# Kernel tuning notes

Hardware: AMD Instinct MI355X
Metric: run time of the kernel (lower is better)

The kernel has to match this reference:

```python
import jax, jax.numpy as jnp
import numpy as np

LN2 = 0.6931471805599453

def ssp(x):
    # 'shifted_sp' activation: softplus(x) - log(2)
    return jax.nn.softplus(x) - LN2

def _res_chain(x, W1, b1, W2, b2):
    # PhysNetResidual chain: x <- lin2(ssp(lin1(ssp(x)))) + x
    # W1/W2: [n_res, F, F], b1/b2: [n_res, F]
    for j in range(W1.shape[0]):
        h = ssp(x) @ W1[j] + b1[j]
        x = ssp(h) @ W2[j] + b2[j] + x
    return x

def _physnet_module(feat, radial_aev, idx12, p):
    (W_I, b_I, W_J, b_J, W_gate, gvec, W_int, b_int,
     ri_W1, ri_b1, ri_W2, ri_b2,
     ra_W1, ra_b1, ra_W2, ra_b2,
     ro_W1, ro_b1, ro_W2, ro_b2, W_out, b_out) = p
    N, F = feat.shape
    # self term (no species are dummy -> non_dummy indexing is identity)
    h_self = ssp(ssp(feat) @ W_I + b_I)                       # [N,F]
    # pair messages
    gate = radial_aev @ W_gate                                 # [P,F] (no bias)
    f12 = feat[idx12]                                          # [2,P,F] gather
    fm = ssp(ssp(f12) @ W_J + b_J)                             # [2,P,F]
    pair_msg = gate[None] * fm                                 # [2,P,F]
    proto = jnp.zeros_like(feat).at[idx12.reshape(-1)].add(
        pair_msg.reshape(-1, F))                               # scatter-add
    proto = proto + h_self
    msg = _res_chain(proto, ri_W1, ri_b1, ri_W2, ri_b2)
    feat2 = feat * gvec + ssp(msg) @ W_int + b_int
    feat2 = _res_chain(feat2, ra_W1, ra_b1, ra_W2, ra_b2)
    e = ssp(_res_chain(feat2, ro_W1, ro_b1, ro_W2, ro_b2)) @ W_out + b_out  # [N]
    return e, feat2

def setup_inputs() -> dict:
    key = jax.random.key(0)
    L, F, R = 5, 128, 64
    M, A = 128, 64
    N = M * A
    P = 400000
    ks = jax.random.split(key, 20)
    s = 0.05  # small weight scale keeps activations stable across 5 modules
    inp = {
        'species': jax.random.randint(ks[0], (M, A), 0, 4, dtype=jnp.int32),
        'features': jax.random.normal(ks[1], (N, F), jnp.float32),
        'radial_aev': jax.random.uniform(ks[2], (P, R), jnp.float32),
        'atom_index12': jax.random.randint(ks[3], (2, P), 0, N, dtype=jnp.int32),
        'W_I': jax.random.normal(ks[4], (L, F, F)) * s,
        'b_I': jnp.zeros((L, F)),
        'W_J': jax.random.normal(ks[5], (L, F, F)) * s,
        'b_J': jnp.zeros((L, F)),
        'W_gate': jax.random.normal(ks[6], (L, R, F)) * s,
        'gvec': jnp.ones((L, F)),
        'W_int': jax.random.normal(ks[7], (L, F, F)) * s,
        'b_int': jnp.zeros((L, F)),
        'ri_W1': jax.random.normal(ks[8], (L, 3, F, F)) * s,
        'ri_b1': jnp.zeros((L, 3, F)),
        'ri_W2': jax.random.normal(ks[9], (L, 3, F, F)) * s,
        'ri_b2': jnp.zeros((L, 3, F)),
        'ra_W1': jax.random.normal(ks[10], (L, 2, F, F)) * s,
        'ra_b1': jnp.zeros((L, 2, F)),
        'ra_W2': jax.random.normal(ks[11], (L, 2, F, F)) * s,
        'ra_b2': jnp.zeros((L, 2, F)),
        'ro_W1': jax.random.normal(ks[12], (L, 1, F, F)) * s,
        'ro_b1': jnp.zeros((L, 1, F)),
        'ro_W2': jax.random.normal(ks[13], (L, 1, F, F)) * s,
        'ro_b2': jnp.zeros((L, 1, F)),
        'W_out': jax.random.normal(ks[14], (L, F)) * s,
        'b_out': jnp.zeros((L,)),
    }
    return inp

def reference(species, features, radial_aev, atom_index12,
              W_I, b_I, W_J, b_J, W_gate, gvec, W_int, b_int,
              ri_W1, ri_b1, ri_W2, ri_b2,
              ra_W1, ra_b1, ra_W2, ra_b2,
              ro_W1, ro_b1, ro_W2, ro_b2, W_out, b_out):
    M, A = species.shape
    params = (W_I, b_I, W_J, b_J, W_gate, gvec, W_int, b_int,
              ri_W1, ri_b1, ri_W2, ri_b2,
              ra_W1, ra_b1, ra_W2, ra_b2,
              ro_W1, ro_b1, ro_W2, ro_b2, W_out, b_out)
    feat = features
    energies = jnp.zeros((M * A,), features.dtype)
    for l in range(W_I.shape[0]):  # fixed small module loop
        p = tuple(arr[l] for arr in params)
        e, feat = _physnet_module(feat, radial_aev, atom_index12, p)
        energies = energies + e
    return energies.reshape(M, A), feat
```

## Files before the change

kernel.cpp:

```cpp
#include <hip/hip_runtime.h>


#define LN2F 0.69314718055994530942f
#define NB 128

using short8  = __attribute__((ext_vector_type(8))) short;
using float4v = __attribute__((ext_vector_type(4))) float;
typedef const __attribute__((address_space(1))) unsigned int* gas1_t;
typedef __attribute__((address_space(3))) unsigned int* las3_t;

__device__ __forceinline__ float sspf(float x) {
  float ax = fabsf(x);
  return fmaxf(x, 0.0f) + __logf(1.0f + __expf(-ax)) - LN2F;
}

__device__ __forceinline__ unsigned short f2bf(float x) {
  return (unsigned short)((__float_as_uint(x) + 0x8000u) >> 16);
}

__device__ __forceinline__ unsigned short f2bf_ne(float x) {
  unsigned int u = __float_as_uint(x);
  u += 0x7fffu + ((u >> 16) & 1u);
  return (unsigned short)(u >> 16);
}

__device__ __forceinline__ void dma16(const void* g, void* l) {
  __builtin_amdgcn_global_load_lds((gas1_t)(unsigned long long)g,
                                   (las3_t)(unsigned long long)l, 16, 0, 0);
}

__device__ __forceinline__ void dma32k(const unsigned short* g, unsigned short* l,
                                       int w, int lane) {
  const char* gb = (const char*)g + w * 2048 + lane * 16;
  char* lb = (char*)l + w * 2048;
  dma16(gb, lb);
  dma16(gb + 1024, lb + 1024);
}
__device__ __forceinline__ void dma16k(const unsigned short* g, unsigned short* l,
                                       int w, int lane) {
  dma16((const char*)g + w * 1024 + lane * 16, (char*)l + w * 1024);
}

__global__ __launch_bounds__(256) void hist_pass(const int* __restrict__ idx,
                                                 unsigned int* __restrict__ H,
                                                 int n2p, int C) {
  __shared__ unsigned int h[8192];
  int b = blockIdx.x, tid = threadIdx.x;
  for (int i = tid; i < 8192; i += 256) h[i] = 0;
  __syncthreads();
  int s = b * C, e = min(s + C, n2p);
  for (int i = s + tid; i < e; i += 256) atomicAdd(&h[idx[i]], 1u);
  __syncthreads();
  for (int i = tid; i < 8192; i += 256) H[(size_t)b * 8192 + i] = h[i];
}

__global__ __launch_bounds__(256) void col_scan(unsigned int* __restrict__ H,
                                                unsigned int* __restrict__ tot) {
  int a = blockIdx.x * 256 + threadIdx.x;
  unsigned int run = 0;
  for (int b = 0; b < NB; ++b) {
    unsigned int v = H[(size_t)b * 8192 + a];
    H[(size_t)b * 8192 + a] = run;
    run += v;
  }
  tot[a] = run;
}

__global__ __launch_bounds__(256) void scan_kernel(const unsigned int* __restrict__ cnt,
                                                   unsigned int* __restrict__ off, int NA) {
  int t = threadIdx.x;
  unsigned int local[32], s = 0;
#pragma unroll
  for (int i = 0; i < 32; ++i) { local[i] = cnt[t * 32 + i]; s += local[i]; }
  unsigned int v = s;
  int lane = t & 63, w = t >> 6;
#pragma unroll
  for (int o = 1; o < 64; o <<= 1) {
    unsigned int u = __shfl_up(v, o, 64);
    if (lane >= o) v += u;
  }
  __shared__ unsigned int wt4[4];
  if (lane == 63) wt4[w] = v;
  __syncthreads();
  unsigned int base = 0;
  for (int k = 0; k < w; ++k) base += wt4[k];
  unsigned int excl = base + v - s;
#pragma unroll
  for (int i = 0; i < 32; ++i) { off[t * 32 + i] = excl; excl += local[i]; }
  if (t == 255) off[NA] = excl;
}

__global__ __launch_bounds__(256) void place_pass(const int* __restrict__ idx,
                                                  const unsigned int* __restrict__ H,
                                                  const unsigned int* __restrict__ off,
                                                  unsigned int* __restrict__ pairid,
                                                  int P, int C) {
  __shared__ unsigned int pos[8192];
  int b = blockIdx.x, tid = threadIdx.x;
  for (int i = tid; i < 8192; i += 256)
    pos[i] = off[i] + H[(size_t)b * 8192 + i];
  __syncthreads();
  int n2p = 2 * P;
  int s = b * C, e = min(s + C, n2p);
  for (int i = s + tid; i < e; i += 256) {
    int a = idx[i];
    unsigned int p = atomicAdd(&pos[a], 1u);
    pairid[p] = (i >= P) ? (unsigned int)(i - P) : (unsigned int)i;
  }
}

__global__ __launch_bounds__(256) void gather_kernel(const float* __restrict__ radial,
                                                     const unsigned int* __restrict__ off,
                                                     const unsigned int* __restrict__ pairid,
                                                     float* __restrict__ S) {
  __shared__ float red[3][64];
  int a = blockIdx.x;
  int lane = threadIdx.x & 63, w = threadIdx.x >> 6;
  unsigned int b = off[a], e = off[a + 1];
  float acc = 0.0f;
  for (unsigned int base = b + w; base < e; base += 32) {
    unsigned int pp[8];
    float vv[8];
#pragma unroll
    for (int k = 0; k < 8; ++k) {
      unsigned int j = base + 4 * k;
      pp[k] = pairid[j < e ? j : b];
    }
#pragma unroll
    for (int k = 0; k < 8; ++k) vv[k] = radial[(size_t)pp[k] * 64 + lane];
#pragma unroll
    for (int k = 0; k < 8; ++k) {
      unsigned int j = base + 4 * k;
      acc += (j < e) ? vv[k] : 0.0f;
    }
  }
  if (w > 0) red[w - 1][lane] = acc;
  __syncthreads();
  if (w == 0) {
    acc += red[0][lane] + red[1][lane] + red[2][lane];
    S[(size_t)a * 64 + lane] = acc;
  }
}

struct PrepArgs {
  const float* src[80];
  int isgate[80];
};

__global__ __launch_bounds__(256) void prep_weights(PrepArgs A, unsigned short* __restrict__ Wt) {
  int m = blockIdx.x;
  const float* s = A.src[m];
  unsigned short* d = Wt + (size_t)m * 16384;
  if (!A.isgate[m]) {
    for (int it = 0; it < 8; ++it) {
      int q = threadIdx.x + it * 256;
      int n = q & 127, j = q >> 7;
      unsigned short tmp[8];
#pragma unroll
      for (int cc = 0; cc < 8; ++cc) tmp[cc] = f2bf_ne(s[(8 * j + cc) * 128 + n]);
      *(uint4*)(d + (n * 16 + (j ^ (n & 15))) * 8) = *(uint4*)tmp;
    }
  } else {
    for (int it = 0; it < 4; ++it) {
      int q = threadIdx.x + it * 256;
      int n = q & 127, j = q >> 7;
      unsigned short tmp[8];
#pragma unroll
      for (int cc = 0; cc < 8; ++cc) tmp[cc] = f2bf_ne(s[(8 * j + cc) * 128 + n]);
      *(uint4*)(d + (n * 8 + (j ^ (n & 7))) * 8) = *(uint4*)tmp;
    }
  }
}

struct BiasArgs {
  const float* p[17];
  int stride[17];
  const float* b_out;
};

__global__ __launch_bounds__(256) void pack_bias(BiasArgs B, float* __restrict__ dst) {
  int l = blockIdx.x;
  for (int i = threadIdx.x; i < 17 * 128; i += 256) {
    int s = i >> 7;
    dst[(size_t)l * 2304 + i] = B.p[s][l * B.stride[s] + (i & 127)];
  }
  if (threadIdx.x == 0) dst[(size_t)l * 2304 + 17 * 128] = B.b_out[l];
}

struct ChainArgs {
  const float* feat_in;
  const float* S;
  const unsigned short* wt;
  const float* bias_pack;
  float* feat_out;
  float* energy;
};

__device__ __forceinline__ void gemm128s(const unsigned short* sA_, const unsigned short* sW,
                                         int arow, int col0, int l16, int quad, float4v* acc) {
  const unsigned short* ar = sA_ + (arow + l16) * 136 + quad * 8;
  short8 a0 = *(const short8*)(ar);
  short8 a1 = *(const short8*)(ar + 32);
  short8 a2 = *(const short8*)(ar + 64);
  short8 a3 = *(const short8*)(ar + 96);
  const unsigned short* bb = sW + col0 * 128;
  *acc = __builtin_amdgcn_mfma_f32_16x16x32_bf16(a0, *(const short8*)(bb + ((quad + 0) ^ l16) * 8), *acc, 0, 0, 0);
  *acc = __builtin_amdgcn_mfma_f32_16x16x32_bf16(a1, *(const short8*)(bb + ((quad + 4) ^ l16) * 8), *acc, 0, 0, 0);
  *acc = __builtin_amdgcn_mfma_f32_16x16x32_bf16(a2, *(const short8*)(bb + ((quad + 8) ^ l16) * 8), *acc, 0, 0, 0);
  *acc = __builtin_amdgcn_mfma_f32_16x16x32_bf16(a3, *(const short8*)(bb + ((quad + 12) ^ l16) * 8), *acc, 0, 0, 0);
}

__device__ __forceinline__ void gemm64s(const unsigned short* sS_, const unsigned short* sW,
                                        int arow, int col0, int l16, int quad, float4v* acc) {
  const unsigned short* ar = sS_ + (arow + l16) * 72 + quad * 8;
  short8 a0 = *(const short8*)(ar);
  short8 a1 = *(const short8*)(ar + 32);
  int l8 = l16 & 7;
  const unsigned short* bb = sW + col0 * 64;
  *acc = __builtin_amdgcn_mfma_f32_16x16x32_bf16(a0, *(const short8*)(bb + ((quad + 0) ^ l8) * 8), *acc, 0, 0, 0);
  *acc = __builtin_amdgcn_mfma_f32_16x16x32_bf16(a1, *(const short8*)(bb + ((quad + 4) ^ l8) * 8), *acc, 0, 0, 0);
}

__device__ __forceinline__ void write_ssp_A(unsigned short* sA_, const float4v v,
                                            int arow, int col0, int quad) {
#pragma unroll
  for (int r = 0; r < 4; ++r)
    sA_[(arow + quad * 4 + r) * 136 + col0] = f2bf(sspf(v[r]));
}

__global__ __launch_bounds__(1024, 4) void chain_kernel(ChainArgs A) {
  __shared__ __align__(16) unsigned short swb[2][16384];
  __shared__ __align__(16) unsigned short sA[2][32 * 136];
  __shared__ __align__(16) unsigned short sS[32 * 72];
  __shared__ float sBias[2304];
  __shared__ float sE[32];

  const int tid  = threadIdx.x;
  const int row0 = blockIdx.x * 32;
  const int lane = tid & 63;
  const int w    = tid >> 6;
  const int g    = w >> 3;
  const int c    = w & 7;
  const int l16  = lane & 15;
  const int quad = lane >> 4;
  const int arow = 16 * g;
  const int col0 = 16 * c + l16;

  dma16k(A.wt, swb[0], w, lane);

  for (int i = tid; i < 32 * 64; i += 1024) {
    int r = i >> 6, k = i & 63;
    sS[r * 72 + k] = f2bf(A.S[(size_t)(row0 + r) * 64 + k]);
  }
  for (int i = tid; i < 32 * 128; i += 1024) {
    int r = i >> 7, k = i & 127;
    sA[0][r * 136 + k] = f2bf(sspf(A.feat_in[(size_t)(row0 + r) * 128 + k]));
  }
  float4v ff;
#pragma unroll
  for (int r = 0; r < 4; ++r)
    ff[r] = A.feat_in[(size_t)(row0 + arow + quad * 4 + r) * 128 + col0];
  if (tid < 32) sE[tid] = 0.0f;
  __syncthreads();

  const float4v Z = {0.f, 0.f, 0.f, 0.f};
  float4v gG, fm, xf, t4;
  float p0 = 0.f, p1 = 0.f, p2 = 0.f, p3 = 0.f, bsum = 0.f;

#pragma unroll 1
  for (int l = 0; l < 5; ++l) {
    const size_t slot0 = (size_t)l * 16 * 16384;

    dma32k(A.wt + slot0 + 16384, swb[1], w, lane);
    for (int i = tid; i < 2304; i += 1024) sBias[i] = A.bias_pack[(size_t)l * 2304 + i];
    gG = Z;
    gemm64s(sS, swb[0], arow, col0, l16, quad, &gG);
    __syncthreads();

    dma32k(A.wt + slot0 + 2 * 16384, swb[0], w, lane);
    fm = Z;
    gemm128s(sA[0], swb[1], arow, col0, l16, quad, &fm);
    {
      float bv = sBias[0 * 128 + col0];
#pragma unroll
      for (int r = 0; r < 4; ++r) fm[r] = sspf(fm[r] + bv);
    }
    __syncthreads();

    dma32k(A.wt + slot0 + 3 * 16384, swb[1], w, lane);
    t4 = Z;
    gemm128s(sA[0], swb[0], arow, col0, l16, quad, &t4);
    {
      float bv = sBias[1 * 128 + col0];
#pragma unroll
      for (int r = 0; r < 4; ++r) xf[r] = fm[r] * gG[r] + sspf(t4[r] + bv);
    }
    write_ssp_A(sA[1], xf, arow, col0, quad);
    __syncthreads();

#pragma unroll
    for (int jj = 0; jj < 3; ++jj) {
      const int th = 3 + 2 * jj;
      dma32k(A.wt + slot0 + (size_t)(th + 1) * 16384, swb[th & 1 ? 0 : 1], w, lane);
      t4 = Z;
      gemm128s(sA[1], swb[th & 1], arow, col0, l16, quad, &t4);
      {
        float bv = sBias[(th - 1) * 128 + col0];
#pragma unroll
        for (int r = 0; r < 4; ++r) t4[r] += bv;
      }
      write_ssp_A(sA[0], t4, arow, col0, quad);
      __syncthreads();

      const int tx = th + 1;
      dma32k(A.wt + slot0 + (size_t)(tx + 1) * 16384, swb[tx & 1 ? 0 : 1], w, lane);
      t4 = Z;
      gemm128s(sA[0], swb[tx & 1], arow, col0, l16, quad, &t4);
      {
        float bv = sBias[(tx - 1) * 128 + col0];
#pragma unroll
        for (int r = 0; r < 4; ++r) xf[r] += t4[r] + bv;
      }
      write_ssp_A(sA[1], xf, arow, col0, quad);
      __syncthreads();
    }

    dma32k(A.wt + slot0 + 10 * 16384, swb[0], w, lane);
    t4 = Z;
    gemm128s(sA[1], swb[1], arow, col0, l16, quad, &t4);
    {
      float bv = sBias[8 * 128 + col0];
      float gv = sBias[15 * 128 + col0];
#pragma unroll
      for (int r = 0; r < 4; ++r) xf[r] = ff[r] * gv + t4[r] + bv;
    }
    write_ssp_A(sA[0], xf, arow, col0, quad);
    __syncthreads();

#pragma unroll
    for (int jj = 0; jj < 2; ++jj) {
      const int th = 10 + 2 * jj;
      dma32k(A.wt + slot0 + (size_t)(th + 1) * 16384, swb[th & 1 ? 0 : 1], w, lane);
      t4 = Z;
      gemm128s(sA[0], swb[th & 1], arow, col0, l16, quad, &t4);
      {
        float bv = sBias[(th - 1) * 128 + col0];
#pragma unroll
        for (int r = 0; r < 4; ++r) t4[r] += bv;
      }
      write_ssp_A(sA[1], t4, arow, col0, quad);
      __syncthreads();

      const int tx = th + 1;
      dma32k(A.wt + slot0 + (size_t)(tx + 1) * 16384, swb[tx & 1 ? 0 : 1], w, lane);
      t4 = Z;
      gemm128s(sA[1], swb[tx & 1], arow, col0, l16, quad, &t4);
      {
        float bv = sBias[(tx - 1) * 128 + col0];
#pragma unroll
        for (int r = 0; r < 4; ++r) xf[r] += t4[r] + bv;
      }
      write_ssp_A(sA[0], xf, arow, col0, quad);
      __syncthreads();
    }

    ff = xf;
    if (l == 4) {
#pragma unroll
      for (int r = 0; r < 4; ++r)
        A.feat_out[(size_t)(row0 + arow + quad * 4 + r) * 128 + col0] = xf[r];
    }

    dma32k(A.wt + slot0 + 15 * 16384, swb[1], w, lane);
    t4 = Z;
    gemm128s(sA[0], swb[0], arow, col0, l16, quad, &t4);
    {
      float bv = sBias[13 * 128 + col0];
#pragma unroll
      for (int r = 0; r < 4; ++r) t4[r] += bv;
    }
    write_ssp_A(sA[1], t4, arow, col0, quad);
    __syncthreads();

    if (l < 4) dma16k(A.wt + slot0 + 16 * 16384, swb[0], w, lane);
    t4 = Z;
    gemm128s(sA[1], swb[1], arow, col0, l16, quad, &t4);
    {
      float bv = sBias[14 * 128 + col0];
      float wv = sBias[16 * 128 + col0];
      p0 += sspf(xf[0] + t4[0] + bv) * wv;
      p1 += sspf(xf[1] + t4[1] + bv) * wv;
      p2 += sspf(xf[2] + t4[2] + bv) * wv;
      p3 += sspf(xf[3] + t4[3] + bv) * wv;
    }
    bsum += sBias[17 * 128];
    __syncthreads();
  }

#pragma unroll
  for (int o = 1; o < 16; o <<= 1) {
    p0 += __shfl_xor(p0, o, 64);
    p1 += __shfl_xor(p1, o, 64);
    p2 += __shfl_xor(p2, o, 64);
    p3 += __shfl_xor(p3, o, 64);
  }
  if (l16 == 0) {
    atomicAdd(&sE[arow + quad * 4 + 0], p0);
    atomicAdd(&sE[arow + quad * 4 + 1], p1);
    atomicAdd(&sE[arow + quad * 4 + 2], p2);
    atomicAdd(&sE[arow + quad * 4 + 3], p3);
  }
  __syncthreads();
  if (tid < 32) A.energy[row0 + tid] = sE[tid] + bsum;
}

extern "C" void kernel_launch(void* const* d_in, const int* in_sizes, int n_in,
                              void* d_out, int out_size, void* d_ws, size_t ws_size,
                              hipStream_t stream) {
  const float* features = (const float*)d_in[1];
  const float* radial   = (const float*)d_in[2];
  const int*   idx12    = (const int*)  d_in[3];
  const float* W_I    = (const float*)d_in[4];
  const float* b_I    = (const float*)d_in[5];
  const float* W_J    = (const float*)d_in[6];
  const float* b_J    = (const float*)d_in[7];
  const float* W_gate = (const float*)d_in[8];
  const float* gvec   = (const float*)d_in[9];
  const float* W_int  = (const float*)d_in[10];
  const float* b_int  = (const float*)d_in[11];
  const float* ri_W1  = (const float*)d_in[12];
  const float* ri_b1  = (const float*)d_in[13];
  const float* ri_W2  = (const float*)d_in[14];
  const float* ri_b2  = (const float*)d_in[15];
  const float* ra_W1  = (const float*)d_in[16];
  const float* ra_b1  = (const float*)d_in[17];
  const float* ra_W2  = (const float*)d_in[18];
  const float* ra_b2  = (const float*)d_in[19];
  const float* ro_W1  = (const float*)d_in[20];
  const float* ro_b1  = (const float*)d_in[21];
  const float* ro_W2  = (const float*)d_in[22];
  const float* ro_b2  = (const float*)d_in[23];
  const float* W_out  = (const float*)d_in[24];
  const float* b_out  = (const float*)d_in[25];

  const int N = in_sizes[1] / 128;
  const int P = in_sizes[3] / 2;
  const int L = in_sizes[25];
  const int n2p = 2 * P;
  const int C = (n2p + NB - 1) / NB;

  float* S = (float*)d_ws;
  float* bias_pack = S + (size_t)N * 64;
  unsigned short* Wt = (unsigned short*)(bias_pack + 5 * 2304);
  unsigned int* H      = (unsigned int*)(Wt + (size_t)80 * 16384);
  unsigned int* tot    = H + (size_t)NB * 8192;
  unsigned int* off    = tot + N;
  unsigned int* pairid = off + N + 4;

  PrepArgs pa;
  for (int l = 0; l < L; ++l) {
    const float* fx[16] = {
      W_gate + l * 8192,
      W_J + l * 16384, W_I + l * 16384,
      ri_W1 + (l * 3 + 0) * 16384, ri_W2 + (l * 3 + 0) * 16384,
      ri_W1 + (l * 3 + 1) * 16384, ri_W2 + (l * 3 + 1) * 16384,
      ri_W1 + (l * 3 + 2) * 16384, ri_W2 + (l * 3 + 2) * 16384,
      W_int + l * 16384,
      ra_W1 + (l * 2 + 0) * 16384, ra_W2 + (l * 2 + 0) * 16384,
      ra_W1 + (l * 2 + 1) * 16384, ra_W2 + (l * 2 + 1) * 16384,
      ro_W1 + l * 16384, ro_W2 + l * 16384 };
    for (int t = 0; t < 16; ++t) { pa.src[l * 16 + t] = fx[t]; pa.isgate[l * 16 + t] = (t == 0); }
  }
  prep_weights<<<80, 256, 0, stream>>>(pa, Wt);

  BiasArgs ba;
  const float* bp[17] = { b_J, b_I,
    ri_b1, ri_b2, ri_b1 + 128, ri_b2 + 128, ri_b1 + 256, ri_b2 + 256,
    b_int, ra_b1, ra_b2, ra_b1 + 128, ra_b2 + 128, ro_b1, ro_b2, gvec, W_out };
  int st[17] = {128,128, 384,384,384,384,384,384, 128, 256,256,256,256, 128,128,128,128};
  for (int q = 0; q < 17; ++q) { ba.p[q] = bp[q]; ba.stride[q] = st[q]; }
  ba.b_out = b_out;
  pack_bias<<<5, 256, 0, stream>>>(ba, bias_pack);

  hist_pass<<<NB, 256, 0, stream>>>(idx12, H, n2p, C);
  col_scan<<<32, 256, 0, stream>>>(H, tot);
  scan_kernel<<<1, 256, 0, stream>>>(tot, off, N);
  place_pass<<<NB, 256, 0, stream>>>(idx12, H, off, pairid, P, C);
  gather_kernel<<<N, 256, 0, stream>>>(radial, off, pairid, S);

  ChainArgs ca;
  ca.feat_in   = features;
  ca.S         = S;
  ca.wt        = Wt;
  ca.bias_pack = bias_pack;
  ca.energy    = (float*)d_out;
  ca.feat_out  = (float*)d_out + N;
  chain_kernel<<<N / 32, 1024, 0, stream>>>(ca);
}
```

Measured before the change: 347.3 us.

## Halve chain-kernel row tile, read biases from global, vectorize radial gather

The chain kernel now processes 16 atoms per block with 8 waves instead of 32 atoms with 16 waves, so twice as many blocks each stream the full weight set via LDS DMA. Each wave's share of every weight-tile copy doubles. Per-layer bias staging into shared memory is removed and biases are read directly from global memory per column. The gather kernel switches to float4 loads with 16 lanes per pair and a shuffle reduction. The smaller tile means more blocks and more parallelism, at the cost of twice the total weight traffic from L2.

```diff
diff --git a/kernel.cpp b/kernel.cpp
--- a/kernel.cpp
+++ b/kernel.cpp
@@ -29,16 +29,21 @@
                                    (las3_t)(unsigned long long)l, 16, 0, 0);
 }
 
-__device__ __forceinline__ void dma32k(const unsigned short* g, unsigned short* l,
-                                       int w, int lane) {
+__device__ __forceinline__ void dma32k8(const unsigned short* g, unsigned short* l,
+                                        int w, int lane) {
+  const char* gb = (const char*)g + w * 4096 + lane * 16;
+  char* lb = (char*)l + w * 4096;
+  dma16(gb, lb);
+  dma16(gb + 1024, lb + 1024);
+  dma16(gb + 2048, lb + 2048);
+  dma16(gb + 3072, lb + 3072);
+}
+__device__ __forceinline__ void dma16k8(const unsigned short* g, unsigned short* l,
+                                        int w, int lane) {
   const char* gb = (const char*)g + w * 2048 + lane * 16;
   char* lb = (char*)l + w * 2048;
   dma16(gb, lb);
   dma16(gb + 1024, lb + 1024);
-}
-__device__ __forceinline__ void dma16k(const unsigned short* g, unsigned short* l,
-                                       int w, int lane) {
-  dma16((const char*)g + w * 1024 + lane * 16, (char*)l + w * 1024);
 }
 
 __global__ __launch_bounds__(256) void hist_pass(const int* __restrict__ idx,
@@ -113,32 +118,41 @@
                                                      const unsigned int* __restrict__ off,
                                                      const unsigned int* __restrict__ pairid,
                                                      float* __restrict__ S) {
-  __shared__ float red[3][64];
+  __shared__ float4v red[3][16];
   int a = blockIdx.x;
   int lane = threadIdx.x & 63, w = threadIdx.x >> 6;
+  int grp = lane >> 4, l16v = lane & 15;
   unsigned int b = off[a], e = off[a + 1];
-  float acc = 0.0f;
-  for (unsigned int base = b + w; base < e; base += 32) {
+  float4v acc = {0.f, 0.f, 0.f, 0.f};
+  for (unsigned int base = b; base < e; base += 128) {
     unsigned int pp[8];
-    float vv[8];
 #pragma unroll
     for (int k = 0; k < 8; ++k) {
-      unsigned int j = base + 4 * k;
+      unsigned int j = base + k * 16 + w * 4 + grp;
       pp[k] = pairid[j < e ? j : b];
     }
-#pragma unroll
-    for (int k = 0; k < 8; ++k) vv[k] = radial[(size_t)pp[k] * 64 + lane];
+    float4v vv[8];
+#pragma unroll
+    for (int k = 0; k < 8; ++k)
+      vv[k] = *(const float4v*)(radial + (size_t)pp[k] * 64 + l16v * 4);
 #pragma unroll
     for (int k = 0; k < 8; ++k) {
-      unsigned int j = base + 4 * k;
-      acc += (j < e) ? vv[k] : 0.0f;
-    }
-  }
-  if (w > 0) red[w - 1][lane] = acc;
-  __syncthreads();
-  if (w == 0) {
-    acc += red[0][lane] + red[1][lane] + red[2][lane];
-    S[(size_t)a * 64 + lane] = acc;
+      unsigned int j = base + k * 16 + w * 4 + grp;
+      if (j < e) acc += vv[k];
+    }
+  }
+#pragma unroll
+  for (int o = 16; o < 64; o <<= 1) {
+#pragma unroll
+    for (int cc = 0; cc < 4; ++cc) acc[cc] += __shfl_xor(acc[cc], o, 64);
+  }
+  if (w > 0 && grp == 0) red[w - 1][l16v] = acc;
+  __syncthreads();
+  if (w == 0 && grp == 0) {
+    acc += red[0][l16v];
+    acc += red[1][l16v];
+    acc += red[2][l16v];
+    *(float4v*)(S + (size_t)a * 64 + l16v * 4) = acc;
   }
 }
 
@@ -197,8 +211,8 @@
 };
 
 __device__ __forceinline__ void gemm128s(const unsigned short* sA_, const unsigned short* sW,
-                                         int arow, int col0, int l16, int quad, float4v* acc) {
-  const unsigned short* ar = sA_ + (arow + l16) * 136 + quad * 8;
+                                         int col0, int l16, int quad, float4v* acc) {
+  const unsigned short* ar = sA_ + l16 * 136 + quad * 8;
   short8 a0 = *(const short8*)(ar);
   short8 a1 = *(const short8*)(ar + 32);
   short8 a2 = *(const short8*)(ar + 64);
@@ -211,8 +225,8 @@
 }
 
 __device__ __forceinline__ void gemm64s(const unsigned short* sS_, const unsigned short* sW,
-                                        int arow, int col0, int l16, int quad, float4v* acc) {
-  const unsigned short* ar = sS_ + (arow + l16) * 72 + quad * 8;
+                                        int col0, int l16, int quad, float4v* acc) {
+  const unsigned short* ar = sS_ + l16 * 72 + quad * 8;
   short8 a0 = *(const short8*)(ar);
   short8 a1 = *(const short8*)(ar + 32);
   int l8 = l16 & 7;
@@ -222,45 +236,42 @@
 }
 
 __device__ __forceinline__ void write_ssp_A(unsigned short* sA_, const float4v v,
-                                            int arow, int col0, int quad) {
+                                            int col0, int quad) {
 #pragma unroll
   for (int r = 0; r < 4; ++r)
-    sA_[(arow + quad * 4 + r) * 136 + col0] = f2bf(sspf(v[r]));
-}
-
-__global__ __launch_bounds__(1024, 4) void chain_kernel(ChainArgs A) {
+    sA_[(quad * 4 + r) * 136 + col0] = f2bf(sspf(v[r]));
+}
+
+__global__ __launch_bounds__(512, 4) void chain_kernel(ChainArgs A) {
   __shared__ __align__(16) unsigned short swb[2][16384];
-  __shared__ __align__(16) unsigned short sA[2][32 * 136];
-  __shared__ __align__(16) unsigned short sS[32 * 72];
-  __shared__ float sBias[2304];
-  __shared__ float sE[32];
+  __shared__ __align__(16) unsigned short sA[2][16 * 136];
+  __shared__ __align__(16) unsigned short sS[16 * 72];
+  __shared__ float sE[16];
 
   const int tid  = threadIdx.x;
-  const int row0 = blockIdx.x * 32;
+  const int row0 = blockIdx.x * 16;
   const int lane = tid & 63;
   const int w    = tid >> 6;
-  const int g    = w >> 3;
-  const int c    = w & 7;
   const int l16  = lane & 15;
   const int quad = lane >> 4;
-  const int arow = 16 * g;
-  const int col0 = 16 * c + l16;
-
-  dma16k(A.wt, swb[0], w, lane);
-
-  for (int i = tid; i < 32 * 64; i += 1024) {
+  const int col0 = 16 * w + l16;
+  const float* bcol = A.bias_pack + col0;
+
+  dma16k8(A.wt, swb[0], w, lane);
+
+  for (int i = tid; i < 16 * 64; i += 512) {
     int r = i >> 6, k = i & 63;
     sS[r * 72 + k] = f2bf(A.S[(size_t)(row0 + r) * 64 + k]);
   }
-  for (int i = tid; i < 32 * 128; i += 1024) {
+  for (int i = tid; i < 16 * 128; i += 512) {
     int r = i >> 7, k = i & 127;
     sA[0][r * 136 + k] = f2bf(sspf(A.feat_in[(size_t)(row0 + r) * 128 + k]));
   }
   float4v ff;
 #pragma unroll
   for (int r = 0; r < 4; ++r)
-    ff[r] = A.feat_in[(size_t)(row0 + arow + quad * 4 + r) * 128 + col0];
-  if (tid < 32) sE[tid] = 0.0f;
+    ff[r] = A.feat_in[(size_t)(row0 + quad * 4 + r) * 128 + col0];
+  if (tid < 16) sE[tid] = 0.0f;
   __syncthreads();
 
   const float4v Z = {0.f, 0.f, 0.f, 0.f};
@@ -270,97 +281,97 @@
 #pragma unroll 1
   for (int l = 0; l < 5; ++l) {
     const size_t slot0 = (size_t)l * 16 * 16384;
-
-    dma32k(A.wt + slot0 + 16384, swb[1], w, lane);
-    for (int i = tid; i < 2304; i += 1024) sBias[i] = A.bias_pack[(size_t)l * 2304 + i];
+    const float* bl = bcol + l * 2304;
+
+    dma32k8(A.wt + slot0 + 16384, swb[1], w, lane);
     gG = Z;
-    gemm64s(sS, swb[0], arow, col0, l16, quad, &gG);
+    gemm64s(sS, swb[0], col0, l16, quad, &gG);
     __syncthreads();
 
-    dma32k(A.wt + slot0 + 2 * 16384, swb[0], w, lane);
-    fm = Z;
-    gemm128s(sA[0], swb[1], arow, col0, l16, quad, &fm);
     {
-      float bv = sBias[0 * 128 + col0];
+      float bv = bl[0 * 128];
+      dma32k8(A.wt + slot0 + 2 * 16384, swb[0], w, lane);
+      fm = Z;
+      gemm128s(sA[0], swb[1], col0, l16, quad, &fm);
 #pragma unroll
       for (int r = 0; r < 4; ++r) fm[r] = sspf(fm[r] + bv);
     }
     __syncthreads();
 
-    dma32k(A.wt + slot0 + 3 * 16384, swb[1], w, lane);
-    t4 = Z;
-    gemm128s(sA[0], swb[0], arow, col0, l16, quad, &t4);
     {
-      float bv = sBias[1 * 128 + col0];
+      float bv = bl[1 * 128];
+      dma32k8(A.wt + slot0 + 3 * 16384, swb[1], w, lane);
+      t4 = Z;
+      gemm128s(sA[0], swb[0], col0, l16, quad, &t4);
 #pragma unroll
       for (int r = 0; r < 4; ++r) xf[r] = fm[r] * gG[r] + sspf(t4[r] + bv);
     }
-    write_ssp_A(sA[1], xf, arow, col0, quad);
+    write_ssp_A(sA[1], xf, col0, quad);
     __syncthreads();
 
 #pragma unroll
     for (int jj = 0; jj < 3; ++jj) {
       const int th = 3 + 2 * jj;
-      dma32k(A.wt + slot0 + (size_t)(th + 1) * 16384, swb[th & 1 ? 0 : 1], w, lane);
-      t4 = Z;
-      gemm128s(sA[1], swb[th & 1], arow, col0, l16, quad, &t4);
       {
-        float bv = sBias[(th - 1) * 128 + col0];
+        float bv = bl[(th - 1) * 128];
+        dma32k8(A.wt + slot0 + (size_t)(th + 1) * 16384, swb[th & 1 ? 0 : 1], w, lane);
+        t4 = Z;
+        gemm128s(sA[1], swb[th & 1], col0, l16, quad, &t4);
 #pragma unroll
         for (int r = 0; r < 4; ++r) t4[r] += bv;
       }
-      write_ssp_A(sA[0], t4, arow, col0, quad);
+      write_ssp_A(sA[0], t4, col0, quad);
       __syncthreads();
 
       const int tx = th + 1;
-      dma32k(A.wt + slot0 + (size_t)(tx + 1) * 16384, swb[tx & 1 ? 0 : 1], w, lane);
-      t4 = Z;
-      gemm128s(sA[0], swb[tx & 1], arow, col0, l16, quad, &t4);
       {
-        float bv = sBias[(tx - 1) * 128 + col0];
+        float bv = bl[(tx - 1) * 128];
+        dma32k8(A.wt + slot0 + (size_t)(tx + 1) * 16384, swb[tx & 1 ? 0 : 1], w, lane);
+        t4 = Z;
+        gemm128s(sA[0], swb[tx & 1], col0, l16, quad, &t4);
 #pragma unroll
         for (int r = 0; r < 4; ++r) xf[r] += t4[r] + bv;
       }
-      write_ssp_A(sA[1], xf, arow, col0, quad);
+      write_ssp_A(sA[1], xf, col0, quad);
       __syncthreads();
     }
 
-    dma32k(A.wt + slot0 + 10 * 16384, swb[0], w, lane);
-    t4 = Z;
-    gemm128s(sA[1], swb[1], arow, col0, l16, quad, &t4);
     {
-      float bv = sBias[8 * 128 + col0];
-      float gv = sBias[15 * 128 + col0];
+      float bv = bl[8 * 128];
+      float gv = bl[15 * 128];
+      dma32k8(A.wt + slot0 + 10 * 16384, swb[0], w, lane);
+      t4 = Z;
+      gemm128s(sA[1], swb[1], col0, l16, quad, &t4);
 #pragma unroll
       for (int r = 0; r < 4; ++r) xf[r] = ff[r] * gv + t4[r] + bv;
     }
-    write_ssp_A(sA[0], xf, arow, col0, quad);
+    write_ssp_A(sA[0], xf, col0, quad);
     __syncthreads();
 
 #pragma unroll
     for (int jj = 0; jj < 2; ++jj) {
       const int th = 10 + 2 * jj;
-      dma32k(A.wt + slot0 + (size_t)(th + 1) * 16384, swb[th & 1 ? 0 : 1], w, lane);
-      t4 = Z;
-      gemm128s(sA[0], swb[th & 1], arow, col0, l16, quad, &t4);
       {
-        float bv = sBias[(th - 1) * 128 + col0];
+        float bv = bl[(th - 1) * 128];
+        dma32k8(A.wt + slot0 + (size_t)(th + 1) * 16384, swb[th & 1 ? 0 : 1], w, lane);
+        t4 = Z;
+        gemm128s(sA[0], swb[th & 1], col0, l16, quad, &t4);
 #pragma unroll
         for (int r = 0; r < 4; ++r) t4[r] += bv;
       }
-      write_ssp_A(sA[1], t4, arow, col0, quad);
+      write_ssp_A(sA[1], t4, col0, quad);
       __syncthreads();
 
       const int tx = th + 1;
-      dma32k(A.wt + slot0 + (size_t)(tx + 1) * 16384, swb[tx & 1 ? 0 : 1], w, lane);
-      t4 = Z;
-      gemm128s(sA[1], swb[tx & 1], arow, col0, l16, quad, &t4);
       {
-        float bv = sBias[(tx - 1) * 128 + col0];
+        float bv = bl[(tx - 1) * 128];
+        dma32k8(A.wt + slot0 + (size_t)(tx + 1) * 16384, swb[tx & 1 ? 0 : 1], w, lane);
+        t4 = Z;
+        gemm128s(sA[1], swb[tx & 1], col0, l16, quad, &t4);
 #pragma unroll
         for (int r = 0; r < 4; ++r) xf[r] += t4[r] + bv;
       }
-      write_ssp_A(sA[0], xf, arow, col0, quad);
+      write_ssp_A(sA[0], xf, col0, quad);
       __syncthreads();
     }
 
@@ -368,32 +379,32 @@
     if (l == 4) {
 #pragma unroll
       for (int r = 0; r < 4; ++r)
-        A.feat_out[(size_t)(row0 + arow + quad * 4 + r) * 128 + col0] = xf[r];
-    }
-
-    dma32k(A.wt + slot0 + 15 * 16384, swb[1], w, lane);
-    t4 = Z;
-    gemm128s(sA[0], swb[0], arow, col0, l16, quad, &t4);
+        A.feat_out[(size_t)(row0 + quad * 4 + r) * 128 + col0] = xf[r];
+    }
+
     {
-      float bv = sBias[13 * 128 + col0];
+      float bv = bl[13 * 128];
+      dma32k8(A.wt + slot0 + 15 * 16384, swb[1], w, lane);
+      t4 = Z;
+      gemm128s(sA[0], swb[0], col0, l16, quad, &t4);
 #pragma unroll
       for (int r = 0; r < 4; ++r) t4[r] += bv;
     }
-    write_ssp_A(sA[1], t4, arow, col0, quad);
+    write_ssp_A(sA[1], t4, col0, quad);
     __syncthreads();
 
-    if (l < 4) dma16k(A.wt + slot0 + 16 * 16384, swb[0], w, lane);
-    t4 = Z;
-    gemm128s(sA[1], swb[1], arow, col0, l16, quad, &t4);
     {
-      float bv = sBias[14 * 128 + col0];
-      float wv = sBias[16 * 128 + col0];
+      float bv = bl[14 * 128];
+      float wv = bl[16 * 128];
+      if (l < 4) dma16k8(A.wt + slot0 + 16 * 16384, swb[0], w, lane);
+      t4 = Z;
+      gemm128s(sA[1], swb[1], col0, l16, quad, &t4);
       p0 += sspf(xf[0] + t4[0] + bv) * wv;
       p1 += sspf(xf[1] + t4[1] + bv) * wv;
       p2 += sspf(xf[2] + t4[2] + bv) * wv;
       p3 += sspf(xf[3] + t4[3] + bv) * wv;
     }
-    bsum += sBias[17 * 128];
+    bsum += A.bias_pack[l * 2304 + 17 * 128];
     __syncthreads();
   }
 
@@ -405,13 +416,13 @@
     p3 += __shfl_xor(p3, o, 64);
   }
   if (l16 == 0) {
-    atomicAdd(&sE[arow + quad * 4 + 0], p0);
-    atomicAdd(&sE[arow + quad * 4 + 1], p1);
-    atomicAdd(&sE[arow + quad * 4 + 2], p2);
-    atomicAdd(&sE[arow + quad * 4 + 3], p3);
-  }
-  __syncthreads();
-  if (tid < 32) A.energy[row0 + tid] = sE[tid] + bsum;
+    atomicAdd(&sE[quad * 4 + 0], p0);
+    atomicAdd(&sE[quad * 4 + 1], p1);
+    atomicAdd(&sE[quad * 4 + 2], p2);
+    atomicAdd(&sE[quad * 4 + 3], p3);
+  }
+  __syncthreads();
+  if (tid < 16) A.energy[row0 + tid] = sE[tid] + bsum;
 }
 
 extern "C" void kernel_launch(void* const* d_in, const int* in_sizes, int n_in,
@@ -495,5 +506,5 @@
   ca.bias_pack = bias_pack;
   ca.energy    = (float*)d_out;
   ca.feat_out  = (float*)d_out + N;
-  chain_kernel<<<N / 32, 1024, 0, stream>>>(ca);
-}
+  chain_kernel<<<N / 16, 512, 0, stream>>>(ca);
+}
```

Result: no change. 352.6 us (+1.5%).
